# Performance work log

Hardware: AMD Instinct MI355X
Metric: run time of the kernel (lower is better)

Reference implementation:

```python
import jax, jax.numpy as jnp
import numpy as np

B, S, IN, H, OUT = 32, 512, 1024, 1024, 1024


def setup_inputs() -> dict:
    key = jax.random.key(0)
    ks = jax.random.split(key, 12)
    sc = 0.02
    d = {
        "x": jax.random.normal(ks[0], (B, S, IN), dtype=jnp.float32),
        # torch nn.Linear weights are (out_features, in_features); in_features = IN + H
        "Wf": jax.random.normal(ks[1], (H, IN + H), dtype=jnp.float32) * sc,
        "bf": jax.random.normal(ks[2], (H,), dtype=jnp.float32) * sc,
        "Wi": jax.random.normal(ks[3], (H, IN + H), dtype=jnp.float32) * sc,
        "bi": jax.random.normal(ks[4], (H,), dtype=jnp.float32) * sc,
        "Wc": jax.random.normal(ks[5], (H, IN + H), dtype=jnp.float32) * sc,
        "bc": jax.random.normal(ks[6], (H,), dtype=jnp.float32) * sc,
        "Wo": jax.random.normal(ks[7], (H, IN + H), dtype=jnp.float32) * sc,
        "bo": jax.random.normal(ks[8], (H,), dtype=jnp.float32) * sc,
        "Wfc": jax.random.normal(ks[9], (OUT, H), dtype=jnp.float32) * sc,
        "bfc": jax.random.normal(ks[10], (OUT,), dtype=jnp.float32) * sc,
    }
    return d


def reference(x, Wf, bf, Wi, bi, Wc, bc, Wo, bo, Wfc, bfc):
    batch, seq_len, _ = x.shape
    hidden = Wf.shape[0]
    h0 = jnp.zeros((batch, hidden), dtype=x.dtype)
    c0 = jnp.zeros((batch, hidden), dtype=x.dtype)

    def step(carry, x_t):
        h, c = carry
        # NOTE: original concatenates (h_t, x_t) in this order
        z = jnp.concatenate([h, x_t], axis=1)  # [B, H+IN]
        f = jax.nn.sigmoid(z @ Wf.T + bf)
        i = jax.nn.sigmoid(z @ Wi.T + bi)
        c_hat = jnp.tanh(z @ Wc.T + bc)
        c_new = i * c_hat + f * c
        o = jax.nn.sigmoid(z @ Wo.T + bo)
        h_new = o * jnp.tanh(c_new)
        return (h_new, c_new), h_new

    xs = jnp.swapaxes(x, 0, 1)  # [S, B, IN]
    _, hs = jax.lax.scan(step, (h0, c0), xs)  # hs: [S, B, H]
    outputs = jnp.swapaxes(hs, 0, 1)  # [B, S, H]
    out = outputs @ Wfc.T + bfc  # [B, S, OUT]
    return out
```

## Files before the change

kernel.cpp:

```cpp
#include <hip/hip_runtime.h>
#include <hip/hip_bf16.h>

#define BATCH 32
#define SEQ   512
#define IND   1024
#define HD    1024
#define ZD    2048
#define NG    4096
#define WG_ELEMS (1024 * 2048)
#define PBLK 128
#define FSTR 68

typedef short  shortx8 __attribute__((ext_vector_type(8)));
typedef float  floatx4 __attribute__((ext_vector_type(4)));

#define MFMA16(a, b, c) __builtin_amdgcn_mfma_f32_16x16x32_bf16((a), (b), (c), 0, 0, 0)

__device__ __forceinline__ float sigmoidf_(float x) {
    return 1.0f / (1.0f + __expf(-x));
}
__device__ __forceinline__ float tanhf_(float x) {
    return 1.0f - 2.0f / (__expf(2.0f * x) + 1.0f);
}

__device__ __forceinline__ short bf16s(float x) {
    __hip_bfloat16 h = __float2bfloat16(x);
    return *reinterpret_cast<short*>(&h);
}

__device__ __forceinline__ float bf2f(unsigned short u) {
    unsigned v = ((unsigned)u) << 16;
    float f;
    __builtin_memcpy(&f, &v, 4);
    return f;
}

__device__ __forceinline__ shortx8 cvt8(const float* __restrict__ p) {
    float4 v0 = *(const float4*)p;
    float4 v1 = *(const float4*)(p + 4);
    shortx8 r;
    r[0] = bf16s(v0.x); r[1] = bf16s(v0.y); r[2] = bf16s(v0.z); r[3] = bf16s(v0.w);
    r[4] = bf16s(v1.x); r[5] = bf16s(v1.y); r[6] = bf16s(v1.z); r[7] = bf16s(v1.w);
    return r;
}

__global__ __launch_bounds__(256) void cvt_weights(
    const float* __restrict__ Wf, const float* __restrict__ Wi,
    const float* __restrict__ Wc, const float* __restrict__ Wo,
    const float* __restrict__ Wfc,
    __hip_bfloat16* __restrict__ Wb, __hip_bfloat16* __restrict__ Wfcb)
{
    int b = blockIdx.x;
    const float* src;
    __hip_bfloat16* dst;
    if (b < 8192) {
        const int g = b >> 11;
        src = (g == 0) ? Wf : (g == 1) ? Wi : (g == 2) ? Wc : Wo;
        dst = Wb + (size_t)g * WG_ELEMS;
        b &= 2047;
    } else {
        src = Wfc; dst = Wfcb; b -= 8192;
    }
    const int i = (b * 256 + threadIdx.x) * 4;
    float4 v = *(const float4*)(src + i);
    dst[i + 0] = __float2bfloat16(v.x);
    dst[i + 1] = __float2bfloat16(v.y);
    dst[i + 2] = __float2bfloat16(v.z);
    dst[i + 3] = __float2bfloat16(v.w);
}

__global__ __launch_bounds__(256) void gemm_gx(
    const float* __restrict__ x,
    const __hip_bfloat16* __restrict__ Wb,
    const float* __restrict__ bf_, const float* __restrict__ bi_,
    const float* __restrict__ bc_, const float* __restrict__ bo_,
    __hip_bfloat16* __restrict__ Gx, const int t0)
{
    const int wave = (blockIdx.x << 2) + (threadIdx.x >> 6);
    const int mt = wave >> 6;
    const int nt = wave & 63;
    const int lane = threadIdx.x & 63;
    const int quad = lane >> 4;
    const int l16  = lane & 15;
    const int m0 = mt << 6;
    const int n0 = nt << 6;
    const int g  = n0 >> 10;
    const __hip_bfloat16* Wg = Wb + (size_t)g * WG_ELEMS;
    const float* bg = (g == 0) ? bf_ : (g == 1) ? bi_ : (g == 2) ? bc_ : bo_;
    const int j0 = n0 & 1023;

    floatx4 acc[4][4];
#pragma unroll
    for (int i = 0; i < 4; i++)
#pragma unroll
        for (int j = 0; j < 4; j++) acc[i][j] = (floatx4)(0.0f);

    const float* arow[4];
    const __hip_bfloat16* brow[4];
#pragma unroll
    for (int i = 0; i < 4; i++) {
        const int r = m0 + i * 16 + l16;
        const int t = t0 + (r >> 5);
        const int b = r & 31;
        arow[i] = x + ((size_t)b * SEQ + t) * IND + quad * 8;
    }
#pragma unroll
    for (int j = 0; j < 4; j++)
        brow[j] = Wg + (size_t)(j0 + j * 16 + l16) * ZD + HD + quad * 8;

    for (int k0 = 0; k0 < IND; k0 += 32) {
        shortx8 a[4], b[4];
#pragma unroll
        for (int i = 0; i < 4; i++) a[i] = cvt8(arow[i] + k0);
#pragma unroll
        for (int j = 0; j < 4; j++) b[j] = *(const shortx8*)(brow[j] + k0);
#pragma unroll
        for (int i = 0; i < 4; i++)
#pragma unroll
            for (int j = 0; j < 4; j++)
                acc[i][j] = MFMA16(a[i], b[j], acc[i][j]);
    }

#pragma unroll
    for (int j = 0; j < 4; j++) {
        const int n  = n0 + j * 16 + l16;
        const int jj = j0 + j * 16 + l16;
        const float bias = bg[jj];
#pragma unroll
        for (int i = 0; i < 4; i++) {
#pragma unroll
            for (int r = 0; r < 4; r++) {
                const int row = m0 + i * 16 + quad * 4 + r;
                Gx[(size_t)row * NG + n] = __float2bfloat16(acc[i][j][r] + bias);
            }
        }
    }
}

__global__ __launch_bounds__(256) void lstm_step(
    const __hip_bfloat16* __restrict__ gx,
    const int t,
    const __hip_bfloat16* __restrict__ Wb,
    const __hip_bfloat16* __restrict__ hzero,
    float* __restrict__ c,
    __hip_bfloat16* __restrict__ hs)
{
    const int jt = (blockIdx.x << 2) + (threadIdx.x >> 6);
    const int lane = threadIdx.x & 63;
    const int quad = lane >> 4;
    const int l16  = lane & 15;
    const int j0   = jt << 4;

    const __hip_bfloat16* hb;
    size_t rstride;
    if (t == 0) { hb = hzero; rstride = HD; }
    else        { hb = hs + (size_t)(t - 1) * HD; rstride = (size_t)SEQ * HD; }

    const __hip_bfloat16* wrow[4];
#pragma unroll
    for (int g = 0; g < 4; g++)
        wrow[g] = Wb + (size_t)g * WG_ELEMS + (size_t)(j0 + l16) * ZD + quad * 8;

    const __hip_bfloat16* hrow0 = hb + (size_t)l16 * rstride + quad * 8;
    const __hip_bfloat16* hrow1 = hb + (size_t)(16 + l16) * rstride + quad * 8;

    floatx4 acc[4][2];
#pragma unroll
    for (int g = 0; g < 4; g++) { acc[g][0] = (floatx4)(0.0f); acc[g][1] = (floatx4)(0.0f); }

    for (int k0 = 0; k0 < HD; k0 += 32) {
        shortx8 a0 = *(const shortx8*)(hrow0 + k0);
        shortx8 a1 = *(const shortx8*)(hrow1 + k0);
#pragma unroll
        for (int g = 0; g < 4; g++) {
            shortx8 bfrag = *(const shortx8*)(wrow[g] + k0);
            acc[g][0] = MFMA16(a0, bfrag, acc[g][0]);
            acc[g][1] = MFMA16(a1, bfrag, acc[g][1]);
        }
    }

    const int j = j0 + l16;
#pragma unroll
    for (int i = 0; i < 2; i++) {
#pragma unroll
        for (int r = 0; r < 4; r++) {
            const int bb = i * 16 + quad * 4 + r;
            const size_t gbase = (size_t)bb * NG + j;
            const float fp = acc[0][i][r] + __bfloat162float(gx[gbase + 0 * HD]);
            const float ip = acc[1][i][r] + __bfloat162float(gx[gbase + 1 * HD]);
            const float cp = acc[2][i][r] + __bfloat162float(gx[gbase + 2 * HD]);
            const float op = acc[3][i][r] + __bfloat162float(gx[gbase + 3 * HD]);
            const float fg = sigmoidf_(fp);
            const float ig = sigmoidf_(ip);
            const float cg = tanhf_(cp);
            const float og = sigmoidf_(op);
            const size_t ci = (size_t)bb * HD + j;
            const float cnew = ig * cg + fg * c[ci];
            const float hnew = og * tanhf_(cnew);
            c[ci] = cnew;
            hs[((size_t)bb * SEQ + t) * HD + j] = __float2bfloat16(hnew);
        }
    }
}

__global__ __launch_bounds__(256, 1) void lstm_persist(
    const __hip_bfloat16* __restrict__ Wb,
    const float* __restrict__ x,
    __hip_bfloat16* __restrict__ Gx,
    const float* __restrict__ bf_, const float* __restrict__ bi_,
    const float* __restrict__ bc_, const float* __restrict__ bo_,
    const __hip_bfloat16* __restrict__ Wfcb,
    const float* __restrict__ bfc,
    float* __restrict__ out,
    const int T,
    const __hip_bfloat16* __restrict__ hzero,
    float* __restrict__ c_ws,
    __hip_bfloat16* __restrict__ hs,
    unsigned* __restrict__ bar)
{
    __shared__ float accf[2 * 1168];

    const int tid  = threadIdx.x;
    const int blk  = blockIdx.x;
    const int wv   = tid >> 6;
    const int lane = tid & 63;
    const int quad = lane >> 4;
    const int l16  = lane & 15;
    unsigned* gcnt = bar + 128 * FSTR;

    if (blk >= PBLK) {
        const int pb_ = blk - PBLK;
        const int pw = pb_ * 4 + wv;
        {
            const int nt = pw & 63;
            const int n0 = nt << 6;
            const int g  = n0 >> 10;
            const __hip_bfloat16* Wg = Wb + (size_t)g * WG_ELEMS;
            const float* bg = (g == 0) ? bf_ : (g == 1) ? bi_ : (g == 2) ? bc_ : bo_;
            const int j0 = n0 & 1023;

            const __hip_bfloat16* brow[4];
#pragma unroll
            for (int j = 0; j < 4; j++)
                brow[j] = Wg + (size_t)(j0 + j * 16 + l16) * ZD + HD + quad * 8;

            float bias[4];
#pragma unroll
            for (int j = 0; j < 4; j++) bias[j] = bg[j0 + j * 16 + l16];

            for (int it = 0; it < 32; it++) {
                const int mt = (pw >> 6) + 8 * it;
                const int m0 = mt << 6;

                floatx4 acc[4][4];
#pragma unroll
                for (int i = 0; i < 4; i++)
#pragma unroll
                    for (int j = 0; j < 4; j++) acc[i][j] = (floatx4)(0.0f);

                const float* arow[4];
#pragma unroll
                for (int i = 0; i < 4; i++) {
                    const int r = m0 + i * 16 + l16;
                    const int t = r >> 5;
                    const int b = r & 31;
                    arow[i] = x + ((size_t)b * SEQ + t) * IND + quad * 8;
                }

                for (int k0 = 0; k0 < IND; k0 += 32) {
                    shortx8 a[4], b[4];
#pragma unroll
                    for (int i = 0; i < 4; i++) a[i] = cvt8(arow[i] + k0);
#pragma unroll
                    for (int j = 0; j < 4; j++) b[j] = *(const shortx8*)(brow[j] + k0);
#pragma unroll
                    for (int i = 0; i < 4; i++)
#pragma unroll
                        for (int j = 0; j < 4; j++)
                            acc[i][j] = MFMA16(a[i], b[j], acc[i][j]);
                }

#pragma unroll
                for (int j = 0; j < 4; j++) {
                    const int n = n0 + j * 16 + l16;
#pragma unroll
                    for (int i = 0; i < 4; i++) {
#pragma unroll
                        for (int r = 0; r < 4; r++) {
                            const int row = m0 + i * 16 + quad * 4 + r;
                            const float v = acc[i][j][r] + bias[j];
                            const unsigned my = (unsigned)(unsigned short)bf16s(v);
                            const unsigned nb = (unsigned)__shfl_xor((int)my, 1);
                            if ((l16 & 1) == 0) {
                                unsigned* dst = (unsigned*)(Gx + (size_t)row * NG + n);
                                __hip_atomic_store(dst, my | (nb << 16),
                                                   __ATOMIC_RELAXED,
                                                   __HIP_MEMORY_SCOPE_AGENT);
                            }
                        }
                    }
                }
                asm volatile("s_waitcnt vmcnt(0)" ::: "memory");
                if (lane == 0)
                    __hip_atomic_fetch_add(gcnt + (size_t)mt * FSTR, 1u,
                                           __ATOMIC_RELAXED, __HIP_MEMORY_SCOPE_AGENT);
            }
        }

        {
            const int fb  = (pb_ & 7) * 4 + wv;
            const int fnt = pb_ >> 3;
            const int n0  = fnt << 6;

            const __hip_bfloat16* brow[4];
#pragma unroll
            for (int j = 0; j < 4; j++)
                brow[j] = Wfcb + (size_t)(n0 + j * 16 + l16) * HD + quad * 8;
            float biasf[4];
#pragma unroll
            for (int j = 0; j < 4; j++) biasf[j] = bfc[n0 + j * 16 + l16];

            for (int tc = 0; tc < 8; tc++) {
                const unsigned need = (unsigned)((tc + 1) * 64);
                if (wv == 0) {
                    unsigned* p0 = bar + (size_t)lane * FSTR;
                    unsigned* p1 = bar + (size_t)(64 + lane) * FSTR;
                    bool d0 = false, d1 = false;
                    while (true) {
                        if (!d0) d0 = (__hip_atomic_load(p0, __ATOMIC_RELAXED,
                                           __HIP_MEMORY_SCOPE_AGENT) >= need);
                        if (!d1) d1 = (__hip_atomic_load(p1, __ATOMIC_RELAXED,
                                           __HIP_MEMORY_SCOPE_AGENT) >= need);
                        if (__all(d0 && d1)) break;
                        __builtin_amdgcn_s_sleep(8);
                    }
                    asm volatile("" ::: "memory");
                    __builtin_amdgcn_sched_barrier(0);
                }
                __syncthreads();

                const int m0 = fb * SEQ + tc * 64;

                floatx4 acc[4][4];
#pragma unroll
                for (int i = 0; i < 4; i++)
#pragma unroll
                    for (int j = 0; j < 4; j++) acc[i][j] = (floatx4)(0.0f);

                const __hip_bfloat16* arow[4];
#pragma unroll
                for (int i = 0; i < 4; i++)
                    arow[i] = hs + (size_t)(m0 + i * 16 + l16) * HD + quad * 8;

                for (int k0 = 0; k0 < HD; k0 += 32) {
                    shortx8 a[4], b[4];
#pragma unroll
                    for (int i = 0; i < 4; i++) a[i] = *(const shortx8*)(arow[i] + k0);
#pragma unroll
                    for (int j = 0; j < 4; j++) b[j] = *(const shortx8*)(brow[j] + k0);
#pragma unroll
                    for (int i = 0; i < 4; i++)
#pragma unroll
                        for (int j = 0; j < 4; j++)
                            acc[i][j] = MFMA16(a[i], b[j], acc[i][j]);
                }

#pragma unroll
                for (int j = 0; j < 4; j++) {
                    const int n = n0 + j * 16 + l16;
#pragma unroll
                    for (int i = 0; i < 4; i++) {
#pragma unroll
                        for (int r = 0; r < 4; r++) {
                            const int row = m0 + i * 16 + quad * 4 + r;
                            out[(size_t)row * 1024 + n] = acc[i][j][r] + biasf[j];
                        }
                    }
                }
            }
        }
        return;
    }

    const int wm = wv & 1;
    const int wk = wv >> 1;

    shortx8 Bfrag[2][16];
#pragma unroll
    for (int ct = 0; ct < 2; ct++) {
        const int lc = ct * 16 + l16;
        const int jj = lc >> 2, g = lc & 3;
        const __hip_bfloat16* wr =
            Wb + (size_t)g * WG_ELEMS + (size_t)(blk * 8 + jj) * ZD + wk * 512 + quad * 8;
#pragma unroll
        for (int ks = 0; ks < 16; ks++)
            Bfrag[ct][ks] = *(const shortx8*)(wr + ks * 32);
    }

    const int pjj = tid & 7;
    const int pb  = tid >> 3;
    const int pj  = blk * 8 + pjj;
    float creg = c_ws[blk * 256 + tid];

    if (wv == 0) {
        while (__hip_atomic_load(gcnt, __ATOMIC_RELAXED,
                                 __HIP_MEMORY_SCOPE_AGENT) < 64)
            __builtin_amdgcn_s_sleep(1);
        asm volatile("" ::: "memory");
        __builtin_amdgcn_sched_barrier(0);
    }
    __syncthreads();

    unsigned short gxr0, gxr1, gxr2, gxr3;
    {
        const __hip_bfloat16* gx = Gx + (size_t)pb * NG + pj;
        gxr0 = *(const unsigned short*)(gx + 0 * HD);
        gxr1 = *(const unsigned short*)(gx + 1 * HD);
        gxr2 = *(const unsigned short*)(gx + 2 * HD);
        gxr3 = *(const unsigned short*)(gx + 3 * HD);
    }
    int mt_ok = 0;

    unsigned* mywatch = bar + (size_t)(wk * 64 + lane) * FSTR;

    for (int tt = 0; tt < T; tt++) {
        const int t = tt;
        const __hip_bfloat16* hb;
        size_t rstride;
        if (t == 0) { hb = hzero; rstride = HD; }
        else        { hb = hs + (size_t)(t - 1) * HD; rstride = (size_t)SEQ * HD; }

        unsigned short ngxr0 = 0, ngxr1 = 0, ngxr2 = 0, ngxr3 = 0;
        if (tt + 1 < T) {
            const int mtn = (tt + 1) >> 1;
            if (mtn > mt_ok) {
                while (__hip_atomic_load(gcnt + (size_t)mtn * FSTR, __ATOMIC_RELAXED,
                                         __HIP_MEMORY_SCOPE_AGENT) < 64)
                    __builtin_amdgcn_s_sleep(1);
                mt_ok = mtn;
                asm volatile("" ::: "memory");
                __builtin_amdgcn_sched_barrier(0);
            }
            const __hip_bfloat16* gx1 = Gx + ((size_t)(tt + 1) * BATCH + pb) * NG + pj;
            ngxr0 = *(const unsigned short*)(gx1 + 0 * HD);
            ngxr1 = *(const unsigned short*)(gx1 + 1 * HD);
            ngxr2 = *(const unsigned short*)(gx1 + 2 * HD);
            ngxr3 = *(const unsigned short*)(gx1 + 3 * HD);
        }

        if (tt > 0) {
            while (__hip_atomic_load(mywatch, __ATOMIC_RELAXED,
                                     __HIP_MEMORY_SCOPE_AGENT) < (unsigned)tt)
                __builtin_amdgcn_s_sleep(1);
            asm volatile("" ::: "memory");
            __builtin_amdgcn_sched_barrier(0);
        }

        const __hip_bfloat16* arow =
            hb + (size_t)(wm * 16 + l16) * rstride + wk * 512 + quad * 8;
        floatx4 acc0 = (floatx4)(0.0f), acc1 = (floatx4)(0.0f);
#pragma unroll
        for (int ks = 0; ks < 16; ks++) {
            shortx8 av = *(const shortx8*)(arow + ks * 32);
            acc0 = MFMA16(av, Bfrag[0][ks], acc0);
            acc1 = MFMA16(av, Bfrag[1][ks], acc1);
        }

        {
            const int b0 = wm * 16 + quad * 4;
            *(floatx4*)(accf + wk * 1168 + (l16)      * 36 + b0) = acc0;
            *(floatx4*)(accf + wk * 1168 + (16 + l16) * 36 + b0) = acc1;
        }
        __syncthreads();

        {
            const int i0 = (pjj * 4 + 0) * 36 + pb;
            const int i1 = (pjj * 4 + 1) * 36 + pb;
            const int i2 = (pjj * 4 + 2) * 36 + pb;
            const int i3 = (pjj * 4 + 3) * 36 + pb;
            const float fp = accf[i0] + accf[1168 + i0] + bf2f(gxr0);
            const float ip = accf[i1] + accf[1168 + i1] + bf2f(gxr1);
            const float cp = accf[i2] + accf[1168 + i2] + bf2f(gxr2);
            const float op = accf[i3] + accf[1168 + i3] + bf2f(gxr3);
            const float fg = sigmoidf_(fp);
            const float ig = sigmoidf_(ip);
            const float cg = tanhf_(cp);
            const float og = sigmoidf_(op);
            creg = ig * cg + fg * creg;
            const float hnew = og * tanhf_(creg);

            const unsigned my = (unsigned)(unsigned short)bf16s(hnew);
            const unsigned nb = (unsigned)__shfl_xor((int)my, 1);
            if ((tid & 1) == 0) {
                unsigned* dst = (unsigned*)(hs + ((size_t)pb * SEQ + t) * HD + pj);
                const unsigned packed = my | (nb << 16);
                __hip_atomic_store(dst, packed, __ATOMIC_RELAXED,
                                   __HIP_MEMORY_SCOPE_AGENT);
            }
        }

        __syncthreads();
        if (wv == 0 && lane == 0) {
            __hip_atomic_store(bar + (size_t)blk * FSTR, (unsigned)(tt + 1),
                               __ATOMIC_RELAXED, __HIP_MEMORY_SCOPE_AGENT);
        }

        gxr0 = ngxr0; gxr1 = ngxr1; gxr2 = ngxr2; gxr3 = ngxr3;
    }

    c_ws[blk * 256 + tid] = creg;
}

__global__ __launch_bounds__(256) void gemm_fc(
    const __hip_bfloat16* __restrict__ hs,
    const __hip_bfloat16* __restrict__ Wfcb,
    const float* __restrict__ bfc,
    float* __restrict__ out)
{
    const int wave = (blockIdx.x << 2) + (threadIdx.x >> 6);
    const int mt = wave >> 4;
    const int nt = wave & 15;
    const int lane = threadIdx.x & 63;
    const int quad = lane >> 4;
    const int l16  = lane & 15;
    const int m0 = mt << 6;
    const int n0 = nt << 6;

    floatx4 acc[4][4];
#pragma unroll
    for (int i = 0; i < 4; i++)
#pragma unroll
        for (int j = 0; j < 4; j++) acc[i][j] = (floatx4)(0.0f);

    const __hip_bfloat16* arow[4];
    const __hip_bfloat16* brow[4];
#pragma unroll
    for (int i = 0; i < 4; i++)
        arow[i] = hs + (size_t)(m0 + i * 16 + l16) * HD + quad * 8;
#pragma unroll
    for (int j = 0; j < 4; j++)
        brow[j] = Wfcb + (size_t)(n0 + j * 16 + l16) * HD + quad * 8;

    for (int k0 = 0; k0 < HD; k0 += 32) {
        shortx8 a[4], b[4];
#pragma unroll
        for (int i = 0; i < 4; i++) a[i] = *(const shortx8*)(arow[i] + k0);
#pragma unroll
        for (int j = 0; j < 4; j++) b[j] = *(const shortx8*)(brow[j] + k0);
#pragma unroll
        for (int i = 0; i < 4; i++)
#pragma unroll
            for (int j = 0; j < 4; j++)
                acc[i][j] = MFMA16(a[i], b[j], acc[i][j]);
    }

#pragma unroll
    for (int j = 0; j < 4; j++) {
        const int n = n0 + j * 16 + l16;
        const float bias = bfc[n];
#pragma unroll
        for (int i = 0; i < 4; i++) {
#pragma unroll
            for (int r = 0; r < 4; r++) {
                const int row = m0 + i * 16 + quad * 4 + r;
                out[(size_t)row * 1024 + n] = acc[i][j][r] + bias;
            }
        }
    }
}

extern "C" void kernel_launch(void* const* d_in, const int* in_sizes, int n_in,
                              void* d_out, int out_size, void* d_ws, size_t ws_size,
                              hipStream_t stream) {
    const float* x   = (const float*)d_in[0];
    const float* Wf  = (const float*)d_in[1];
    const float* bf_ = (const float*)d_in[2];
    const float* Wi  = (const float*)d_in[3];
    const float* bi_ = (const float*)d_in[4];
    const float* Wc  = (const float*)d_in[5];
    const float* bc_ = (const float*)d_in[6];
    const float* Wo  = (const float*)d_in[7];
    const float* bo_ = (const float*)d_in[8];
    const float* Wfc = (const float*)d_in[9];
    const float* bfc = (const float*)d_in[10];
    float* out = (float*)d_out;

    char* ws = (char*)d_ws;
    const size_t WB_OFF  = 0;
    const size_t WFC_OFF = (size_t)4 * WG_ELEMS * 2;
    const size_t HS_OFF  = WFC_OFF + (size_t)HD * HD * 2;
    const size_t ST_OFF  = HS_OFF + (size_t)BATCH * SEQ * HD * 2;
    const size_t HZ_BYTES  = (size_t)BATCH * HD * 2;
    const size_t C_BYTES   = (size_t)PBLK * 256 * 4;
    const size_t BAR_BYTES = (size_t)(128 + 256) * FSTR * 4;
    const size_t ST_BYTES  = HZ_BYTES + C_BYTES + BAR_BYTES;
    const size_t GX_OFF  = ST_OFF + ST_BYTES;

    __hip_bfloat16* Wb    = (__hip_bfloat16*)(ws + WB_OFF);
    __hip_bfloat16* Wfcb  = (__hip_bfloat16*)(ws + WFC_OFF);
    __hip_bfloat16* hs    = (__hip_bfloat16*)(ws + HS_OFF);
    __hip_bfloat16* hzero = (__hip_bfloat16*)(ws + ST_OFF);
    float*          cbuf  = (float*)(ws + ST_OFF + HZ_BYTES);
    unsigned*       bar   = (unsigned*)(ws + ST_OFF + HZ_BYTES + C_BYTES);
    __hip_bfloat16* Gx    = (__hip_bfloat16*)(ws + GX_OFF);

    const size_t GX_FULL = (size_t)SEQ * BATCH * NG * 2;
    const int persist = (GX_OFF + GX_FULL <= ws_size);
    int T_CHUNK = 1;
    if (!persist) {
        const size_t GX_STEP = (size_t)BATCH * NG * 2;
        const int fopts[3] = {8, 2, 1};
        for (int i = 0; i < 3; i++) {
            if (GX_OFF + (size_t)fopts[i] * GX_STEP <= ws_size) {
                T_CHUNK = fopts[i]; break;
            }
        }
    }

    cvt_weights<<<9216, 256, 0, stream>>>(Wf, Wi, Wc, Wo, Wfc, Wb, Wfcb);

    hipMemsetAsync(ws + ST_OFF, 0, ST_BYTES, stream);

    if (persist) {
        lstm_persist<<<2 * PBLK, 256, 0, stream>>>(
            Wb, x, Gx, bf_, bi_, bc_, bo_, Wfcb, bfc, out,
            SEQ, hzero, cbuf, hs, bar);
    } else {
        for (int t0 = 0; t0 < SEQ; t0 += T_CHUNK) {
            gemm_gx<<<T_CHUNK * 8, 256, 0, stream>>>(
                x, Wb, bf_, bi_, bc_, bo_, Gx, t0);
            for (int t = t0; t < t0 + T_CHUNK; t++) {
                const __hip_bfloat16* gx_t = Gx + (size_t)(t - t0) * BATCH * NG;
                lstm_step<<<16, 256, 0, stream>>>(gx_t, t, Wb, hzero, cbuf, hs);
            }
        }
        gemm_fc<<<1024, 256, 0, stream>>>(hs, Wfcb, bfc, out);
    }
}
```

Measured before the change: 2.389 ms.

## Replace per-step block barrier with per-wave flags and double-buffered accumulator panel

Each wave now publishes its own step-completion flag, after waiting for its global stores, instead of the block doing a second __syncthreads and one thread writing a single flag. Consumers read four adjacent per-wave flags and take their minimum. The LDS accumulator panel is double-buffered by step parity, so the trailing barrier can be dropped without the next step's writes racing the current step's reads. This shortens the critical path of the serial recurrence at the cost of four flag loads per poll and twice the LDS for the panel.

```diff
diff --git a/kernel.cpp b/kernel.cpp
--- a/kernel.cpp
+++ b/kernel.cpp
@@ -33,6 +33,16 @@
     float f;
     __builtin_memcpy(&f, &v, 4);
     return f;
+}
+
+__device__ __forceinline__ unsigned min4flags(const unsigned* p) {
+    const unsigned a = __hip_atomic_load(p + 0, __ATOMIC_RELAXED, __HIP_MEMORY_SCOPE_AGENT);
+    const unsigned b = __hip_atomic_load(p + 1, __ATOMIC_RELAXED, __HIP_MEMORY_SCOPE_AGENT);
+    const unsigned c = __hip_atomic_load(p + 2, __ATOMIC_RELAXED, __HIP_MEMORY_SCOPE_AGENT);
+    const unsigned d = __hip_atomic_load(p + 3, __ATOMIC_RELAXED, __HIP_MEMORY_SCOPE_AGENT);
+    const unsigned ab = a < b ? a : b;
+    const unsigned cd = c < d ? c : d;
+    return ab < cd ? ab : cd;
 }
 
 __device__ __forceinline__ shortx8 cvt8(const float* __restrict__ p) {
@@ -218,7 +228,7 @@
     __hip_bfloat16* __restrict__ hs,
     unsigned* __restrict__ bar)
 {
-    __shared__ float accf[2 * 1168];
+    __shared__ float accf[2][2 * 1168];
 
     const int tid  = threadIdx.x;
     const int blk  = blockIdx.x;
@@ -323,14 +333,12 @@
             for (int tc = 0; tc < 8; tc++) {
                 const unsigned need = (unsigned)((tc + 1) * 64);
                 if (wv == 0) {
-                    unsigned* p0 = bar + (size_t)lane * FSTR;
-                    unsigned* p1 = bar + (size_t)(64 + lane) * FSTR;
+                    const unsigned* p0 = bar + (size_t)lane * FSTR;
+                    const unsigned* p1 = bar + (size_t)(64 + lane) * FSTR;
                     bool d0 = false, d1 = false;
                     while (true) {
-                        if (!d0) d0 = (__hip_atomic_load(p0, __ATOMIC_RELAXED,
-                                           __HIP_MEMORY_SCOPE_AGENT) >= need);
-                        if (!d1) d1 = (__hip_atomic_load(p1, __ATOMIC_RELAXED,
-                                           __HIP_MEMORY_SCOPE_AGENT) >= need);
+                        if (!d0) d0 = (min4flags(p0) >= need);
+                        if (!d1) d1 = (min4flags(p1) >= need);
                         if (__all(d0 && d1)) break;
                         __builtin_amdgcn_s_sleep(8);
                     }
@@ -421,7 +429,7 @@
     }
     int mt_ok = 0;
 
-    unsigned* mywatch = bar + (size_t)(wk * 64 + lane) * FSTR;
+    const unsigned* mywatch = bar + (size_t)(wk * 64 + lane) * FSTR;
 
     for (int tt = 0; tt < T; tt++) {
         const int t = tt;
@@ -449,8 +457,7 @@
         }
 
         if (tt > 0) {
-            while (__hip_atomic_load(mywatch, __ATOMIC_RELAXED,
-                                     __HIP_MEMORY_SCOPE_AGENT) < (unsigned)tt)
+            while (min4flags(mywatch) < (unsigned)tt)
                 __builtin_amdgcn_s_sleep(1);
             asm volatile("" ::: "memory");
             __builtin_amdgcn_sched_barrier(0);
@@ -466,10 +473,11 @@
             acc1 = MFMA16(av, Bfrag[1][ks], acc1);
         }
 
+        float* panel = accf[tt & 1];
         {
             const int b0 = wm * 16 + quad * 4;
-            *(floatx4*)(accf + wk * 1168 + (l16)      * 36 + b0) = acc0;
-            *(floatx4*)(accf + wk * 1168 + (16 + l16) * 36 + b0) = acc1;
+            *(floatx4*)(panel + wk * 1168 + (l16)      * 36 + b0) = acc0;
+            *(floatx4*)(panel + wk * 1168 + (16 + l16) * 36 + b0) = acc1;
         }
         __syncthreads();
 
@@ -478,10 +486,10 @@
             const int i1 = (pjj * 4 + 1) * 36 + pb;
             const int i2 = (pjj * 4 + 2) * 36 + pb;
             const int i3 = (pjj * 4 + 3) * 36 + pb;
-            const float fp = accf[i0] + accf[1168 + i0] + bf2f(gxr0);
-            const float ip = accf[i1] + accf[1168 + i1] + bf2f(gxr1);
-            const float cp = accf[i2] + accf[1168 + i2] + bf2f(gxr2);
-            const float op = accf[i3] + accf[1168 + i3] + bf2f(gxr3);
+            const float fp = panel[i0] + panel[1168 + i0] + bf2f(gxr0);
+            const float ip = panel[i1] + panel[1168 + i1] + bf2f(gxr1);
+            const float cp = panel[i2] + panel[1168 + i2] + bf2f(gxr2);
+            const float op = panel[i3] + panel[1168 + i3] + bf2f(gxr3);
             const float fg = sigmoidf_(fp);
             const float ig = sigmoidf_(ip);
             const float cg = tanhf_(cp);
@@ -499,9 +507,9 @@
             }
         }
 
-        __syncthreads();
-        if (wv == 0 && lane == 0) {
-            __hip_atomic_store(bar + (size_t)blk * FSTR, (unsigned)(tt + 1),
+        asm volatile("s_waitcnt vmcnt(0)" ::: "memory");
+        if (lane == 0) {
+            __hip_atomic_store(bar + (size_t)blk * FSTR + wv, (unsigned)(tt + 1),
                                __ATOMIC_RELAXED, __HIP_MEMORY_SCOPE_AGENT);
         }
 
```

Result: slower. 3.607 ms (+51.0%).
